# Kernel optimization log

Hardware: AMD Instinct MI355X
Metric: run time of the kernel (lower is better)

The kernel has to match this reference:

```python
import jax, jax.numpy as jnp
import numpy as np

N, F_IN, F_OUT = 8192, 256, 256
ALPHA = 0.2  # LeakyReLU negative slope
NEG = -9e15

def setup_inputs() -> dict:
    key = jax.random.key(0)
    k1, k2, k3, k4, k5 = jax.random.split(key, 5)
    h = jax.random.normal(k1, (N, F_IN), dtype=jnp.float32)
    adj = jax.random.randint(k2, (N, N), 0, 2, dtype=jnp.int32)
    W_w = jax.random.normal(k3, (F_IN, F_OUT), dtype=jnp.float32) / np.sqrt(F_IN)
    W_b = jax.random.normal(k4, (F_OUT,), dtype=jnp.float32) * 0.01
    a = jax.random.normal(k5, (2 * F_OUT, 1), dtype=jnp.float32) / np.sqrt(2 * F_OUT)
    return {"h": h, "adj": adj, "W_w": W_w, "W_b": W_b, "a": a}

def reference(h, adj, W_w, W_b, a):
    # Wh: [N, F_OUT]
    Wh = h @ W_w + W_b
    a1 = a[:F_OUT, 0]   # scores for source node i (row)
    a2 = a[F_OUT:, 0]   # scores for target node j (col)
    # e[i,j] = leakyrelu(Wh_i . a1 + Wh_j . a2)  -- separable form of the
    # original repeat/cat construction, identical math without the NxNx2F tensor.
    e = jax.nn.leaky_relu((Wh @ a1)[:, None] + (Wh @ a2)[None, :], negative_slope=ALPHA)
    attention = jnp.where(adj > 0, e, NEG)
    attention = jax.nn.softmax(attention, axis=1)
    # dropout is identity in eval / p=0
    h_prime = attention @ Wh  # [N, F_OUT]
    return h_prime
```

## Files before the change

### kernel.cpp

```cpp
#include <hip/hip_runtime.h>
#include <stdint.h>

#define NN 8192
#define FD 256
#define LOG2E 1.44269504088896340736f
#define SPLIT 4
#define JSLICE (NN / SPLIT)
#define NIT (JSLICE / 32)
#define NADJ (JSLICE / 64)

typedef __attribute__((ext_vector_type(8))) __bf16 bf16x8;
typedef __attribute__((ext_vector_type(4))) float f32x4;
typedef __attribute__((ext_vector_type(4))) int i32x4;

__device__ __forceinline__ unsigned short f2bf(float x) {
    unsigned u = __float_as_uint(x);
    u = u + 0x7fffu + ((u >> 16) & 1u);
    return (unsigned short)(u >> 16);
}
__device__ __forceinline__ bf16x8 ld_bf8(const unsigned short* p) {
    uint4 v = *(const uint4*)p;
    return __builtin_bit_cast(bf16x8, v);
}
__device__ __forceinline__ unsigned pack_trunc2(float a, float b) {
    return __builtin_amdgcn_perm(__float_as_uint(b), __float_as_uint(a), 0x07060302u);
}
__device__ __forceinline__ void async_ld16(const void* g, void* lds) {
    __builtin_amdgcn_global_load_lds(
        (const __attribute__((address_space(1))) void*)g,
        (__attribute__((address_space(3))) void*)lds, 16, 0, 0);
}
__device__ __forceinline__ i32x4 ld_nt_i4(const int* p) {
    return __builtin_nontemporal_load((const i32x4*)p);
}

__global__ __launch_bounds__(256) void wtrans_kernel(const float* __restrict__ W,
                                                     unsigned short* __restrict__ WbT) {
    int idx = blockIdx.x * 256 + threadIdx.x;
    int k = idx >> 8, f = idx & 255;
    WbT[f * 256 + k] = f2bf(W[idx]);
}

__global__ __launch_bounds__(256) void gemm1_kernel(const float* __restrict__ h,
                                                    const unsigned short* __restrict__ WbT,
                                                    const float* __restrict__ bias,
                                                    const float* __restrict__ av,
                                                    unsigned short* __restrict__ PBu,
                                                    float* __restrict__ f1p,
                                                    float* __restrict__ f2p) {
    __shared__ float Wh_s[256 * 33];
    __shared__ float red_s[2 * 8 * 32];
    int t = threadIdx.x;
    int l = t & 63, w = t >> 6;
    int jc = (blockIdx.x & 7) * 32 + (blockIdx.x >> 3);
    int i0 = jc * 32;
    int fbase = w * 64;
    int cl = l & 15, q = l >> 4;

    f32x4 acc[2][4] = {};
    const float* hA0 = h + (size_t)(i0 + cl) * FD;
    const float* hA1 = h + (size_t)(i0 + 16 + cl) * FD;

    #pragma unroll
    for (int ks = 0; ks < 8; ++ks) {
        int kk = ks * 32 + q * 8;
        union { unsigned short u[8]; bf16x8 v; } ua0, ua1;
        float4 x0 = *(const float4*)(hA0 + kk);
        float4 x1 = *(const float4*)(hA0 + kk + 4);
        float4 y0 = *(const float4*)(hA1 + kk);
        float4 y1 = *(const float4*)(hA1 + kk + 4);
        ua0.u[0]=f2bf(x0.x); ua0.u[1]=f2bf(x0.y); ua0.u[2]=f2bf(x0.z); ua0.u[3]=f2bf(x0.w);
        ua0.u[4]=f2bf(x1.x); ua0.u[5]=f2bf(x1.y); ua0.u[6]=f2bf(x1.z); ua0.u[7]=f2bf(x1.w);
        ua1.u[0]=f2bf(y0.x); ua1.u[1]=f2bf(y0.y); ua1.u[2]=f2bf(y0.z); ua1.u[3]=f2bf(y0.w);
        ua1.u[4]=f2bf(y1.x); ua1.u[5]=f2bf(y1.y); ua1.u[6]=f2bf(y1.z); ua1.u[7]=f2bf(y1.w);
        #pragma unroll
        for (int bg = 0; bg < 4; ++bg) {
            bf16x8 bF = ld_bf8(WbT + (fbase + bg * 16 + cl) * 256 + kk);
            acc[0][bg] = __builtin_amdgcn_mfma_f32_16x16x32_bf16(ua0.v, bF, acc[0][bg], 0, 0, 0);
            acc[1][bg] = __builtin_amdgcn_mfma_f32_16x16x32_bf16(ua1.v, bF, acc[1][bg], 0, 0, 0);
        }
    }

    #pragma unroll
    for (int mt = 0; mt < 2; ++mt)
        #pragma unroll
        for (int bg = 0; bg < 4; ++bg)
            #pragma unroll
            for (int e = 0; e < 4; ++e) {
                int il = mt * 16 + q * 4 + e;
                int fl = fbase + bg * 16 + cl;
                Wh_s[fl * 33 + il] = acc[mt][bg][e] + bias[fl];
            }
    __syncthreads();
    {
        size_t jcBase = (size_t)jc * 8192;
        #pragma unroll
        for (int u = 0; u < 4; ++u) {
            int fg = u * 4 + (t >> 6);
            int ll = t & 63;
            int c2 = ll & 15, q2 = ll >> 4;
            const float* src = &Wh_s[(fg * 16 + c2) * 33 + q2 * 8];
            union { unsigned short us[8]; uint4 v; } p;
            #pragma unroll
            for (int e = 0; e < 8; ++e) p.us[e] = f2bf(src[e]);
            *(uint4*)(PBu + jcBase + fg * 512 + ll * 8) = p.v;
        }
    }
    {
        int i = t & 31, fc = t >> 5;
        float s1 = 0.f, s2 = 0.f;
        #pragma unroll
        for (int fo = 0; fo < 32; ++fo) {
            int f = fc * 32 + fo;
            float wv = Wh_s[f * 33 + i];
            s1 += wv * av[f];
            s2 += wv * av[256 + f];
        }
        red_s[fc * 32 + i] = s1;
        red_s[256 + fc * 32 + i] = s2;
    }
    __syncthreads();
    if (t < 32) {
        float s = 0.f;
        #pragma unroll
        for (int fc = 0; fc < 8; ++fc) s += red_s[fc * 32 + t];
        f1p[i0 + t] = s * LOG2E;
    } else if (t < 64) {
        int i = t - 32;
        float s = 0.f;
        #pragma unroll
        for (int fc = 0; fc < 8; ++fc) s += red_s[256 + fc * 32 + i];
        f2p[i0 + i] = s * LOG2E;
    }
}

__global__ __launch_bounds__(256, 4) void gat_kernel(const int* __restrict__ adj,
                                                     const unsigned short* __restrict__ PBu,
                                                     const float* __restrict__ f1p,
                                                     const float* __restrict__ f2p,
                                                     float* __restrict__ num,
                                                     float* __restrict__ den) {
    __shared__ __align__(16) unsigned short Bs[2][8192];
    __shared__ unsigned mask_b[4][64];
    __shared__ float f2_s[JSLICE];

    int t = threadIdx.x;
    int l = t & 63, w = t >> 6;
    int s = blockIdx.x & (SPLIT - 1);
    int strip = blockIdx.x / SPLIT;
    int i0b = strip * 64;
    int j0 = s * JSLICE;
    int jw0 = j0 / 32;
    int cl = l & 15, q = l >> 4;

    #pragma unroll
    for (int k = 0; k < JSLICE / 1024; ++k)
        *(float4*)&f2_s[k * 1024 + t * 4] = *(const float4*)(f2p + j0 + k * 1024 + t * 4);

    const char* pbBase = (const char*)(PBu + (size_t)jw0 * 8192);
    #pragma unroll
    for (int k = 0; k < 4; ++k)
        async_ld16(pbBase + k * 4096 + t * 16, (char*)&Bs[0][0] + k * 4096 + t * 16);

    const int* abase = adj + (size_t)(i0b + w * 16 + (l >> 4)) * NN + j0 + (l & 15) * 4;
    i32x4 A0 = ld_nt_i4(abase + 0 * 4 * NN);
    i32x4 A1 = ld_nt_i4(abase + 1 * 4 * NN);
    i32x4 A2 = ld_nt_i4(abase + 2 * 4 * NN);
    i32x4 A3 = ld_nt_i4(abase + 3 * 4 * NN);

    float f1v = f1p[i0b + w * 16 + cl];

    __syncthreads();

    {
        int word = (l >> 3) & 1;
        int sh = 4 * (l & 7);
        int rsub = l >> 4;
        #pragma unroll
        for (int ld = 0; ld < 4; ++ld) {
            i32x4 A = ld == 0 ? A0 : ld == 1 ? A1 : ld == 2 ? A2 : A3;
            unsigned n = (unsigned)(A[0] > 0) | ((unsigned)(A[1] > 0) << 1)
                       | ((unsigned)(A[2] > 0) << 2) | ((unsigned)(A[3] > 0) << 3);
            unsigned v = n << sh;
            v |= __shfl_xor(v, 1);
            v |= __shfl_xor(v, 2);
            v |= __shfl_xor(v, 4);
            if ((l & 7) == 0)
                mask_b[word][w * 16 + ld * 4 + rsub] = v;
        }
    }

    const bf16x8 onesB = __builtin_bit_cast(bf16x8,
        make_uint4(0x3F803F80u, 0x3F803F80u, 0x3F803F80u, 0x3F803F80u));

    f32x4 acc[16] = {};
    f32x4 accR = {};

    #pragma unroll 1
    for (int g = 0; g < NIT; ++g) {
        __syncthreads();

        if (g + 1 < NIT) {
            const char* src = pbBase + (size_t)(g + 1) * 16384;
            char* dst = (char*)&Bs[(g + 1) & 1][0];
            #pragma unroll
            for (int k = 0; k < 4; ++k)
                async_ld16(src + k * 4096 + t * 16, dst + k * 4096 + t * 16);
        }

        if ((g & 1) == 0) {
            int c1 = g / 2 + 1;
            if (c1 < NADJ) {
                int jo = c1 * 64;
                A0 = ld_nt_i4(abase + 0 * 4 * NN + jo);
                A1 = ld_nt_i4(abase + 1 * 4 * NN + jo);
                A2 = ld_nt_i4(abase + 2 * 4 * NN + jo);
                A3 = ld_nt_i4(abase + 3 * 4 * NN + jo);
            }
        } else {
            int c1 = (g + 1) / 2;
            if (c1 < NADJ) {
                int word = (l >> 3) & 1;
                int slot = (g + 1 + word) & 3;
                int sh = 4 * (l & 7);
                int rsub = l >> 4;
                #pragma unroll
                for (int ld = 0; ld < 4; ++ld) {
                    i32x4 A = ld == 0 ? A0 : ld == 1 ? A1 : ld == 2 ? A2 : A3;
                    unsigned n = (unsigned)(A[0] > 0) | ((unsigned)(A[1] > 0) << 1)
                               | ((unsigned)(A[2] > 0) << 2) | ((unsigned)(A[3] > 0) << 3);
                    unsigned v = n << sh;
                    v |= __shfl_xor(v, 1);
                    v |= __shfl_xor(v, 2);
                    v |= __shfl_xor(v, 4);
                    if ((l & 7) == 0)
                        mask_b[slot][w * 16 + ld * 4 + rsub] = v;
                }
            }
        }

        unsigned mw = mask_b[g & 3][w * 16 + cl];
        float4 F0 = *(const float4*)&f2_s[g * 32 + q * 8];
        float4 F1 = *(const float4*)&f2_s[g * 32 + q * 8 + 4];

        unsigned bits = mw >> (q * 8);
        float fe[8] = {F0.x, F0.y, F0.z, F0.w, F1.x, F1.y, F1.z, F1.w};
        float wv[8];
        #pragma unroll
        for (int e = 0; e < 8; ++e) {
            float sv = f1v + fe[e];
            sv = fmaxf(sv, 0.2f * sv);
            float x = __builtin_amdgcn_exp2f(sv);
            x = (bits >> e) & 1 ? x : 0.f;
            wv[e] = x;
        }
        union { unsigned uu[4]; bf16x8 v; } af;
        af.uu[0] = pack_trunc2(wv[0], wv[1]);
        af.uu[1] = pack_trunc2(wv[2], wv[3]);
        af.uu[2] = pack_trunc2(wv[4], wv[5]);
        af.uu[3] = pack_trunc2(wv[6], wv[7]);

        const unsigned short* bu = &Bs[g & 1][0] + l * 8;
        #pragma unroll
        for (int fg = 0; fg < 16; ++fg) {
            bf16x8 B = ld_bf8(bu + fg * 512);
            acc[fg] = __builtin_amdgcn_mfma_f32_16x16x32_bf16(af.v, B, acc[fg], 0, 0, 0);
        }
        accR = __builtin_amdgcn_mfma_f32_16x16x32_bf16(af.v, onesB, accR, 0, 0, 0);
    }

    if (cl == 0) {
        #pragma unroll
        for (int e = 0; e < 4; ++e)
            den[(size_t)s * NN + i0b + w * 16 + q * 4 + e] = accR[e];
    }

    float* nrow = num + (size_t)s * NN * FD;
    #pragma unroll
    for (int e = 0; e < 4; ++e) {
        int r = i0b + w * 16 + q * 4 + e;
        #pragma unroll
        for (int fg = 0; fg < 16; ++fg)
            nrow[(size_t)r * FD + fg * 16 + cl] = acc[fg][e];
    }
}

__global__ __launch_bounds__(256) void combine_kernel(const float* __restrict__ num,
                                                      const float* __restrict__ den,
                                                      float* __restrict__ out) {
    int idx = blockIdx.x * 256 + threadIdx.x;
    int i = idx >> 8;
    float nsum = 0.f, dsum = 0.f;
    #pragma unroll
    for (int s = 0; s < SPLIT; ++s) {
        nsum += num[(size_t)s * NN * FD + idx];
        dsum += den[(size_t)s * NN + i];
    }
    out[idx] = nsum / dsum;
}

extern "C" void kernel_launch(void* const* d_in, const int* in_sizes, int n_in,
                              void* d_out, int out_size, void* d_ws, size_t ws_size,
                              hipStream_t stream) {
    const float* h   = (const float*)d_in[0];
    const int*   adj = (const int*)d_in[1];
    const float* W   = (const float*)d_in[2];
    const float* b   = (const float*)d_in[3];
    const float* a   = (const float*)d_in[4];
    float* out = (float*)d_out;

    char* ws = (char*)d_ws;
    unsigned short* PBu = (unsigned short*)ws;
    unsigned short* WbT = (unsigned short*)(ws + (4u << 20));
    float* f1p = (float*)(ws + (4u << 20) + (128u << 10));
    float* f2p = f1p + NN;
    float* den = f2p + NN;
    float* num = (float*)(ws + (24u << 20));

    wtrans_kernel<<<256, 256, 0, stream>>>(W, WbT);
    gemm1_kernel<<<256, 256, 0, stream>>>(h, WbT, b, a, PBu, f1p, f2p);
    gat_kernel<<<128 * SPLIT, 256, 0, stream>>>(adj, PBu, f1p, f2p, num, den);
    combine_kernel<<<NN * FD / 256, 256, 0, stream>>>(num, den, out);
}
```

Before: 419.4 us.

## Halve j-split and use 512-thread blocks splitting feature columns across wave pairs

```diff
diff --git a/kernel.cpp b/kernel.cpp
--- a/kernel.cpp
+++ b/kernel.cpp
@@ -4,7 +4,7 @@
 #define NN 8192
 #define FD 256
 #define LOG2E 1.44269504088896340736f
-#define SPLIT 4
+#define SPLIT 2
 #define JSLICE (NN / SPLIT)
 #define NIT (JSLICE / 32)
 #define NADJ (JSLICE / 64)
@@ -134,7 +134,7 @@
     }
 }
 
-__global__ __launch_bounds__(256, 4) void gat_kernel(const int* __restrict__ adj,
+__global__ __launch_bounds__(512, 2) void gat_kernel(const int* __restrict__ adj,
                                                      const unsigned short* __restrict__ PBu,
                                                      const float* __restrict__ f1p,
                                                      const float* __restrict__ f2p,
@@ -152,23 +152,23 @@
     int j0 = s * JSLICE;
     int jw0 = j0 / 32;
     int cl = l & 15, q = l >> 4;
-
-    #pragma unroll
-    for (int k = 0; k < JSLICE / 1024; ++k)
-        *(float4*)&f2_s[k * 1024 + t * 4] = *(const float4*)(f2p + j0 + k * 1024 + t * 4);
+    int rgrp = w >> 1;
+    int fh = w & 1;
+
+    #pragma unroll
+    for (int k = 0; k < 2; ++k)
+        *(float4*)&f2_s[k * 2048 + t * 4] = *(const float4*)(f2p + j0 + k * 2048 + t * 4);
 
     const char* pbBase = (const char*)(PBu + (size_t)jw0 * 8192);
     #pragma unroll
-    for (int k = 0; k < 4; ++k)
-        async_ld16(pbBase + k * 4096 + t * 16, (char*)&Bs[0][0] + k * 4096 + t * 16);
-
-    const int* abase = adj + (size_t)(i0b + w * 16 + (l >> 4)) * NN + j0 + (l & 15) * 4;
-    i32x4 A0 = ld_nt_i4(abase + 0 * 4 * NN);
-    i32x4 A1 = ld_nt_i4(abase + 1 * 4 * NN);
-    i32x4 A2 = ld_nt_i4(abase + 2 * 4 * NN);
-    i32x4 A3 = ld_nt_i4(abase + 3 * 4 * NN);
-
-    float f1v = f1p[i0b + w * 16 + cl];
+    for (int k = 0; k < 2; ++k)
+        async_ld16(pbBase + k * 8192 + t * 16, (char*)&Bs[0][0] + k * 8192 + t * 16);
+
+    const int* abase = adj + (size_t)(i0b + w * 8 + (l >> 4)) * NN + j0 + (l & 15) * 4;
+    i32x4 A0 = ld_nt_i4(abase);
+    i32x4 A1 = ld_nt_i4(abase + 4 * NN);
+
+    float f1v = f1p[i0b + rgrp * 16 + cl];
 
     __syncthreads();
 
@@ -177,8 +177,8 @@
         int sh = 4 * (l & 7);
         int rsub = l >> 4;
         #pragma unroll
-        for (int ld = 0; ld < 4; ++ld) {
-            i32x4 A = ld == 0 ? A0 : ld == 1 ? A1 : ld == 2 ? A2 : A3;
+        for (int ld = 0; ld < 2; ++ld) {
+            i32x4 A = ld == 0 ? A0 : A1;
             unsigned n = (unsigned)(A[0] > 0) | ((unsigned)(A[1] > 0) << 1)
                        | ((unsigned)(A[2] > 0) << 2) | ((unsigned)(A[3] > 0) << 3);
             unsigned v = n << sh;
@@ -186,14 +186,14 @@
             v |= __shfl_xor(v, 2);
             v |= __shfl_xor(v, 4);
             if ((l & 7) == 0)
-                mask_b[word][w * 16 + ld * 4 + rsub] = v;
+                mask_b[word][w * 8 + ld * 4 + rsub] = v;
         }
     }
 
     const bf16x8 onesB = __builtin_bit_cast(bf16x8,
         make_uint4(0x3F803F80u, 0x3F803F80u, 0x3F803F80u, 0x3F803F80u));
 
-    f32x4 acc[16] = {};
+    f32x4 acc[8] = {};
     f32x4 accR = {};
 
     #pragma unroll 1
@@ -204,18 +204,16 @@
             const char* src = pbBase + (size_t)(g + 1) * 16384;
             char* dst = (char*)&Bs[(g + 1) & 1][0];
             #pragma unroll
-            for (int k = 0; k < 4; ++k)
-                async_ld16(src + k * 4096 + t * 16, dst + k * 4096 + t * 16);
+            for (int k = 0; k < 2; ++k)
+                async_ld16(src + k * 8192 + t * 16, dst + k * 8192 + t * 16);
         }
 
         if ((g & 1) == 0) {
             int c1 = g / 2 + 1;
             if (c1 < NADJ) {
                 int jo = c1 * 64;
-                A0 = ld_nt_i4(abase + 0 * 4 * NN + jo);
-                A1 = ld_nt_i4(abase + 1 * 4 * NN + jo);
-                A2 = ld_nt_i4(abase + 2 * 4 * NN + jo);
-                A3 = ld_nt_i4(abase + 3 * 4 * NN + jo);
+                A0 = ld_nt_i4(abase + jo);
+                A1 = ld_nt_i4(abase + 4 * NN + jo);
             }
         } else {
             int c1 = (g + 1) / 2;
@@ -225,8 +223,8 @@
                 int sh = 4 * (l & 7);
                 int rsub = l >> 4;
                 #pragma unroll
-                for (int ld = 0; ld < 4; ++ld) {
-                    i32x4 A = ld == 0 ? A0 : ld == 1 ? A1 : ld == 2 ? A2 : A3;
+                for (int ld = 0; ld < 2; ++ld) {
+                    i32x4 A = ld == 0 ? A0 : A1;
                     unsigned n = (unsigned)(A[0] > 0) | ((unsigned)(A[1] > 0) << 1)
                                | ((unsigned)(A[2] > 0) << 2) | ((unsigned)(A[3] > 0) << 3);
                     unsigned v = n << sh;
@@ -234,12 +232,12 @@
                     v |= __shfl_xor(v, 2);
                     v |= __shfl_xor(v, 4);
                     if ((l & 7) == 0)
-                        mask_b[slot][w * 16 + ld * 4 + rsub] = v;
+                        mask_b[slot][w * 8 + ld * 4 + rsub] = v;
                 }
             }
         }
 
-        unsigned mw = mask_b[g & 3][w * 16 + cl];
+        unsigned mw = mask_b[g & 3][rgrp * 16 + cl];
         float4 F0 = *(const float4*)&f2_s[g * 32 + q * 8];
         float4 F1 = *(const float4*)&f2_s[g * 32 + q * 8 + 4];
 
@@ -262,26 +260,27 @@
 
         const unsigned short* bu = &Bs[g & 1][0] + l * 8;
         #pragma unroll
-        for (int fg = 0; fg < 16; ++fg) {
-            bf16x8 B = ld_bf8(bu + fg * 512);
-            acc[fg] = __builtin_amdgcn_mfma_f32_16x16x32_bf16(af.v, B, acc[fg], 0, 0, 0);
-        }
-        accR = __builtin_amdgcn_mfma_f32_16x16x32_bf16(af.v, onesB, accR, 0, 0, 0);
-    }
-
-    if (cl == 0) {
+        for (int b = 0; b < 8; ++b) {
+            bf16x8 B = ld_bf8(bu + (fh * 8 + b) * 512);
+            acc[b] = __builtin_amdgcn_mfma_f32_16x16x32_bf16(af.v, B, acc[b], 0, 0, 0);
+        }
+        if (fh == 0)
+            accR = __builtin_amdgcn_mfma_f32_16x16x32_bf16(af.v, onesB, accR, 0, 0, 0);
+    }
+
+    if (fh == 0 && cl == 0) {
         #pragma unroll
         for (int e = 0; e < 4; ++e)
-            den[(size_t)s * NN + i0b + w * 16 + q * 4 + e] = accR[e];
+            den[(size_t)s * NN + i0b + rgrp * 16 + q * 4 + e] = accR[e];
     }
 
     float* nrow = num + (size_t)s * NN * FD;
     #pragma unroll
     for (int e = 0; e < 4; ++e) {
-        int r = i0b + w * 16 + q * 4 + e;
-        #pragma unroll
-        for (int fg = 0; fg < 16; ++fg)
-            nrow[(size_t)r * FD + fg * 16 + cl] = acc[fg][e];
+        int r = i0b + rgrp * 16 + q * 4 + e;
+        #pragma unroll
+        for (int b = 0; b < 8; ++b)
+            nrow[(size_t)r * FD + (fh * 8 + b) * 16 + cl] = acc[b][e];
     }
 }
 
@@ -319,6 +318,6 @@
 
     wtrans_kernel<<<256, 256, 0, stream>>>(W, WbT);
     gemm1_kernel<<<256, 256, 0, stream>>>(h, WbT, b, a, PBu, f1p, f2p);
-    gat_kernel<<<128 * SPLIT, 256, 0, stream>>>(adj, PBu, f1p, f2p, num, den);
+    gat_kernel<<<128 * SPLIT, 512, 0, stream>>>(adj, PBu, f1p, f2p, num, den);
     combine_kernel<<<NN * FD / 256, 256, 0, stream>>>(num, den, out);
 }
```

Result: slower. 451.7 us (+7.7%).
